# Performance work log

Hardware: AMD Instinct MI355X
Metric: run time of the kernel (lower is better)

## Reference

```python
import jax, jax.numpy as jnp
import numpy as np

# ----- Cl(3,0,1) projective geometric algebra tables (e0^2=0, e1..e3^2=+1) -----
_BLADES = [(), (0,), (1,), (2,), (3,),
           (0, 1), (0, 2), (0, 3), (1, 2), (1, 3), (2, 3),
           (0, 1, 2), (0, 1, 3), (0, 2, 3), (1, 2, 3),
           (0, 1, 2, 3)]
_IDX = {b: i for i, b in enumerate(_BLADES)}

def _blade_mul(a, b):
    lst = list(a) + list(b); sign = 1; n = len(lst)
    for _ in range(n):
        for j in range(n - 1):
            if lst[j] > lst[j + 1]:
                lst[j], lst[j + 1] = lst[j + 1], lst[j]; sign = -sign
    out, i = [], 0
    while i < len(lst):
        if i + 1 < len(lst) and lst[i] == lst[i + 1]:
            if lst[i] == 0:
                return 0, ()
            i += 2
        else:
            out.append(lst[i]); i += 1
    return sign, tuple(out)

_GPn = np.zeros((16, 16, 16), dtype=np.float32)
for _i, _a in enumerate(_BLADES):
    for _j, _b in enumerate(_BLADES):
        _s, _c = _blade_mul(_a, _b)
        if _s:
            _GPn[_i, _j, _IDX[_c]] = _s
GP = jnp.asarray(_GPn)                       # geometric-product structure constants
_gr = np.array([len(b) for b in _BLADES])
_P = np.stack([np.diag((_gr == g).astype(np.float32)) for g in range(5)])  # grade projections
_L0 = _GPn[1].T                               # left-multiplication by e0
BASIS = jnp.asarray(np.concatenate([_P, np.stack([_L0 @ _P[g] for g in range(4)])], 0))  # (9,16,16) equivariant-linear basis
INNER = jnp.asarray(np.array([0.0 if 0 in b else 1.0 for b in _BLADES], np.float32))    # invariant inner-product mask (8 ones)

N_HEADS = 8
_EPS = 1e-6

def equi_linear(mv, s, wmv, wsm, wms, wss):
    # mv: (..., Cin, 16), s: (..., Sin); scalars couple to the grade-0 component
    y_mv = jnp.einsum('oik,kab,...ib->...oa', wmv, BASIS, mv)
    y_mv = y_mv.at[..., 0].add(jnp.einsum('oi,...i->...o', wsm, s))
    y_s = jnp.einsum('oi,...i->...o', wss, s) + jnp.einsum('oi,...i->...o', wms, mv[..., 0])
    return y_mv, y_s

def equi_ln(mv, s):
    f = jnp.mean(jnp.sum(mv * mv * INNER, -1), -1, keepdims=True)  # mean channel norm
    mv = mv / jnp.sqrt(f + _EPS)[..., None]
    s = s / jnp.sqrt(jnp.mean(s * s, -1, keepdims=True) + _EPS)
    return mv, s

def attention(mv, s, wmv, wsm, wms, wss, womv, wosm, woms, woss):
    B, N, C, _ = mv.shape; S = s.shape[-1]; H = N_HEADS
    qkv_mv, qkv_s = equi_linear(mv, s, wmv, wsm, wms, wss)
    q_mv, k_mv, v_mv = [t.reshape(B, N, H, C // H, 16) for t in jnp.split(qkv_mv, 3, axis=-2)]
    q_s, k_s, v_s = [t.reshape(B, N, H, S // H) for t in jnp.split(qkv_s, 3, axis=-1)]
    scale = 1.0 / np.sqrt(8 * (C // H) + S // H)  # 8 invariant comps per mv channel
    scores = (jnp.einsum('bnhci,bmhci->bhnm', q_mv * INNER, k_mv)
              + jnp.einsum('bnhd,bmhd->bhnm', q_s, k_s)) * scale
    a = jax.nn.softmax(scores, axis=-1)
    o_mv = jnp.einsum('bhnm,bmhci->bnhci', a, v_mv).reshape(B, N, C, 16)
    o_s = jnp.einsum('bhnm,bmhd->bnhd', a, v_s).reshape(B, N, S)
    return equi_linear(o_mv, o_s, womv, wosm, woms, woss)

def geo_mlp(mv, s, w1mv, w1sm, w1ms, w1ss, w2mv, w2sm, w2ms, w2ss):
    C = mv.shape[-2]; S = s.shape[-1]
    h_mv, h_s = equi_linear(mv, s, w1mv, w1sm, w1ms, w1ss)  # (...,2C,16), (...,2S)
    gp = jnp.einsum('ijk,...ci,...cj->...ck', GP, h_mv[..., :C, :], h_mv[..., C:, :])
    gp = gp * jax.nn.gelu(gp[..., :1])                       # scalar-gated nonlinearity
    sh = h_s[..., :S] * jax.nn.gelu(h_s[..., S:])
    return equi_linear(gp, sh, w2mv, w2sm, w2ms, w2ss)

def _forward(inputs, win_mv, win_ms, win_bs,
             a_qkv_wmv, a_qkv_wsm, a_qkv_wms, a_qkv_wss,
             a_out_wmv, a_out_wsm, a_out_wms, a_out_wss,
             m1_wmv, m1_wsm, m1_wms, m1_wss,
             m2_wmv, m2_wsm, m2_wms, m2_wss,
             wout_mv, wout_sm):
    B, N, _ = inputs.shape
    # embed_point: coordinates -> trivector components, homogeneous e123 = 1
    mv0 = jnp.zeros((B, N, 1, 16), inputs.dtype)
    mv0 = mv0.at[..., 14].set(1.0)
    mv0 = mv0.at[..., 13].set(-inputs[..., 0:1])
    mv0 = mv0.at[..., 12].set(inputs[..., 1:2])
    mv0 = mv0.at[..., 11].set(-inputs[..., 2:3])
    mv = jnp.einsum('oik,kab,...ib->...oa', win_mv, BASIS, mv0)  # (B,N,C,16)
    s = jnp.einsum('oi,...i->...o', win_ms, mv0[..., 0]) + win_bs  # (B,N,S)
    L = a_qkv_wmv.shape[0]
    for l in range(L):  # loop over structurally-distinct layers only
        n_mv, n_s = equi_ln(mv, s)
        d_mv, d_s = attention(n_mv, n_s, a_qkv_wmv[l], a_qkv_wsm[l], a_qkv_wms[l], a_qkv_wss[l],
                              a_out_wmv[l], a_out_wsm[l], a_out_wms[l], a_out_wss[l])
        mv, s = mv + d_mv, s + d_s
        n_mv, n_s = equi_ln(mv, s)
        d_mv, d_s = geo_mlp(n_mv, n_s, m1_wmv[l], m1_wsm[l], m1_wms[l], m1_wss[l],
                            m2_wmv[l], m2_wsm[l], m2_wms[l], m2_wss[l])
        mv, s = mv + d_mv, s + d_s
    out_mv = jnp.einsum('oik,kab,...ib->...oa', wout_mv, BASIS, mv)  # (B,N,1,16)
    out_mv = out_mv.at[..., 0].add(jnp.einsum('oi,...i->...o', wout_sm, s))
    nodewise = out_mv[..., 0:1]                 # extract_scalar: (B,N,1,1)
    return jnp.mean(nodewise, axis=(-3, -2))    # mean over (points, channels) -> (B,1)

def setup_inputs() -> dict:
    key = jax.random.key(0)
    B, N, C, S, L = 8, 1024, 16, 32, 8
    ks = iter(jax.random.split(key, 32))
    def p(shape, fan):
        return jax.random.normal(next(ks), shape, jnp.float32) / np.sqrt(fan)
    return {
        'inputs': jax.random.normal(next(ks), (B, N, 3), jnp.float32),
        'win_mv': p((C, 1, 9), 9.0),
        'win_ms': p((S, 1), 1.0),
        'win_bs': p((S,), 1.0),
        'a_qkv_wmv': p((L, 3 * C, C, 9), 9.0 * C),
        'a_qkv_wsm': p((L, 3 * C, S), S),
        'a_qkv_wms': p((L, 3 * S, C), C),
        'a_qkv_wss': p((L, 3 * S, S), S),
        'a_out_wmv': p((L, C, C, 9), 9.0 * C),
        'a_out_wsm': p((L, C, S), S),
        'a_out_wms': p((L, S, C), C),
        'a_out_wss': p((L, S, S), S),
        'm1_wmv': p((L, 2 * C, C, 9), 9.0 * C),
        'm1_wsm': p((L, 2 * C, S), S),
        'm1_wms': p((L, 2 * S, C), C),
        'm1_wss': p((L, 2 * S, S), S),
        'm2_wmv': p((L, C, C, 9), 9.0 * C),
        'm2_wsm': p((L, C, S), S),
        'm2_wms': p((L, S, C), C),
        'm2_wss': p((L, S, S), S),
        'wout_mv': p((1, C, 9), 9.0 * C),
        'wout_sm': p((1, S), S),
    }

def reference(inputs, win_mv, win_ms, win_bs,
              a_qkv_wmv, a_qkv_wsm, a_qkv_wms, a_qkv_wss,
              a_out_wmv, a_out_wsm, a_out_wms, a_out_wss,
              m1_wmv, m1_wsm, m1_wms, m1_wss,
              m2_wmv, m2_wsm, m2_wms, m2_wss,
              wout_mv, wout_sm):
    return _forward(inputs, win_mv, win_ms, win_bs,
                    a_qkv_wmv, a_qkv_wsm, a_qkv_wms, a_qkv_wss,
                    a_out_wmv, a_out_wsm, a_out_wms, a_out_wss,
                    m1_wmv, m1_wsm, m1_wms, m1_wss,
                    m2_wmv, m2_wsm, m2_wms, m2_wss,
                    wout_mv, wout_sm)
```

## Files before the change

### kernel.cpp

```cpp
#include <hip/hip_runtime.h>
#include <math.h>

#define BB 8
#define NN 1024
#define LLAYERS 8

typedef unsigned short ushort_t;
typedef unsigned int uint_t;
using bf16x8 = __attribute__((ext_vector_type(8))) short;
using f32x4  = __attribute__((ext_vector_type(4))) float;

__constant__ int d_GRADE[16] = {0,1,1,1,1,2,2,2,2,2,2,3,3,3,3,4};
__constant__ int d_PAIR[16]  = {-1,0,-1,-1,-1,2,3,4,-1,-1,-1,8,9,10,-1,14};
__constant__ int d_IB[8] = {0,2,3,4,8,9,10,14};
__constant__ int d_I2M[16] = {0,1,2,4,8,3,5,9,6,10,12,7,11,13,14,15};
__constant__ int d_M2I[16] = {0,1,2,5,3,6,8,11,4,7,9,12,10,13,14,15};

#define QSCALE (0.22360679774997896f * 1.4426950408889634f)

__device__ __forceinline__ float gelu_tanh(float x) {
  float y = 0.7978845608028654f * (x + 0.044715f * x * x * x);
  float e2 = __builtin_amdgcn_exp2f(y * -2.8853900817779268f);
  return x * __builtin_amdgcn_rcpf(1.0f + e2);
}

__device__ __forceinline__ ushort_t f2b(float f) {
  union { float f; unsigned int u; } x;
  x.f = f;
  unsigned int r = x.u + 0x7fffu + ((x.u >> 16) & 1u);
  return (ushort_t)(r >> 16);
}

__global__ void __launch_bounds__(256) k_embed(
    const float* __restrict__ inp, const float* __restrict__ win_mv,
    const float* __restrict__ win_ms, const float* __restrict__ win_bs,
    float* __restrict__ mv, float* __restrict__ s)
{
  int tok = blockIdx.x, t = threadIdx.x;
  float x = inp[tok * 3 + 0];
  float y = inp[tok * 3 + 1];
  float z = inp[tok * 3 + 2];
  int o = t >> 4, aa = t & 15;
  float ma = (aa == 14) ? 1.f : (aa == 13) ? -x : (aa == 12) ? y : (aa == 11) ? -z : 0.f;
  int g = d_GRADE[aa];
  float val = win_mv[o * 9 + g] * ma;
  int pr = d_PAIR[aa];
  if (pr >= 0) {
    float mp = (pr == 14) ? 1.f : 0.f;
    val += win_mv[o * 9 + 4 + g] * mp;
  }
  mv[(size_t)tok * 256 + t] = val;
  if (t < 32) s[(size_t)tok * 32 + t] = win_bs[t];
  (void)win_ms;
}

__global__ void __launch_bounds__(256) k_ln_qkv(
    const float* __restrict__ mv, const float* __restrict__ s,
    const float* __restrict__ wmv, const float* __restrict__ wsm,
    const float* __restrict__ wms, const float* __restrict__ wss,
    ushort_t* __restrict__ q_bf, ushort_t* __restrict__ k_bf, ushort_t* __restrict__ vT)
{
  __shared__ float pool[9600];
  float* xmv = pool;
  float* xs  = pool + 2048;
  float* yst = pool + 2304;
  float* sst = pool + 8832;

  int t = threadIdx.x;
  int tok0 = blockIdx.x * 8;
  int b = tok0 >> 10, n0 = tok0 & 1023;
  int a = t & 15, og = t >> 4;
  int g = d_GRADE[a], pr = d_PAIR[a];

  float wgq[16], wpq[16], wgk[16], wpk[16], wgv[16], wpv[16];
  #pragma unroll
  for (int i = 0; i < 16; ++i) {
    wgq[i] = wmv[(og)      * 144 + i * 9 + g];
    wgk[i] = wmv[(16 + og) * 144 + i * 9 + g];
    wgv[i] = wmv[(32 + og) * 144 + i * 9 + g];
    wpq[i] = wmv[(og)      * 144 + i * 9 + 4 + g];
    wpk[i] = wmv[(16 + og) * 144 + i * 9 + 4 + g];
    wpv[i] = wmv[(32 + og) * 144 + i * 9 + 4 + g];
  }

  #pragma unroll
  for (int j = 0; j < 2; ++j)
    *(float4*)&xmv[t * 4 + j * 1024] = *(const float4*)&mv[(size_t)tok0 * 256 + t * 4 + j * 1024];
  if (t < 64)
    *(float4*)&xs[t * 4] = *(const float4*)&s[(size_t)tok0 * 32 + t * 4];
  __syncthreads();

  if (t < 128) {
    int tk = t >> 4, ch = t & 15;
    float* xp = &xmv[tk * 256 + ch * 16];
    float4 v0 = *(float4*)&xp[0], v1 = *(float4*)&xp[4];
    float4 v2 = *(float4*)&xp[8], v3 = *(float4*)&xp[12];
    float ss = v0.x*v0.x + v0.z*v0.z + v0.w*v0.w + v1.x*v1.x
             + v2.x*v2.x + v2.y*v2.y + v2.z*v2.z + v3.z*v3.z;
    ss += __shfl_xor(ss, 1); ss += __shfl_xor(ss, 2);
    ss += __shfl_xor(ss, 4); ss += __shfl_xor(ss, 8);
    float inv = rsqrtf(ss / 16.f + 1e-6f);
    v0.x*=inv; v0.y*=inv; v0.z*=inv; v0.w*=inv;
    v1.x*=inv; v1.y*=inv; v1.z*=inv; v1.w*=inv;
    v2.x*=inv; v2.y*=inv; v2.z*=inv; v2.w*=inv;
    v3.x*=inv; v3.y*=inv; v3.z*=inv; v3.w*=inv;
    *(float4*)&xp[0] = v0; *(float4*)&xp[4] = v1;
    *(float4*)&xp[8] = v2; *(float4*)&xp[12] = v3;
    float s0 = xs[tk * 32 + ch * 2], s1 = xs[tk * 32 + ch * 2 + 1];
    float s2 = s0 * s0 + s1 * s1;
    s2 += __shfl_xor(s2, 1); s2 += __shfl_xor(s2, 2);
    s2 += __shfl_xor(s2, 4); s2 += __shfl_xor(s2, 8);
    float sinv = rsqrtf(s2 / 32.f + 1e-6f);
    xs[tk * 32 + ch * 2] = s0 * sinv;
    xs[tk * 32 + ch * 2 + 1] = s1 * sinv;
  }
  __syncthreads();

  for (int tk = 0; tk < 8; ++tk) {
    float y0 = 0.f, y1 = 0.f, y2 = 0.f;
    const float* xb = &xmv[tk * 256];
    #pragma unroll
    for (int i = 0; i < 16; ++i) {
      float xa_ = xb[i * 16 + a];
      y0 += wgq[i] * xa_; y1 += wgk[i] * xa_; y2 += wgv[i] * xa_;
    }
    if (pr >= 0) {
      #pragma unroll
      for (int i = 0; i < 16; ++i) {
        float xp_ = xb[i * 16 + pr];
        y0 += wpq[i] * xp_; y1 += wpk[i] * xp_; y2 += wpv[i] * xp_;
      }
    }
    yst[(tk * 48 + og) * 17 + a] = y0;
    yst[(tk * 48 + 16 + og) * 17 + a] = y1;
    yst[(tk * 48 + 32 + og) * 17 + a] = y2;
  }
  __syncthreads();

  for (int u = t; u < 384; u += 256) {
    int tk = u / 48, o = u % 48;
    float add = 0.f;
    #pragma unroll
    for (int j = 0; j < 32; ++j) add += wsm[o * 32 + j] * xs[tk * 32 + j];
    yst[(tk * 48 + o) * 17 + 0] += add;
  }
  for (int u = t; u < 768; u += 256) {
    int tk = u / 96, o96 = u % 96;
    float yy = 0.f;
    #pragma unroll
    for (int j = 0; j < 32; ++j) yy += wss[o96 * 32 + j] * xs[tk * 32 + j];
    #pragma unroll
    for (int i = 0; i < 16; ++i) yy += wms[o96 * 16 + i] * xmv[tk * 256 + i * 16];
    sst[tk * 96 + o96] = yy;
  }
  __syncthreads();

  if (t < 128) {
    int isK = t >> 6;
    int r = t & 63;
    int tk = r >> 3, h = r & 7;
    float scale = isK ? 1.f : QSCALE;
    const float* base = &yst[(tk * 48 + isK * 16) * 17];
    ushort_t tmp[32];
    #pragma unroll
    for (int j = 0; j < 8; ++j) {
      int blade = d_IB[j];
      tmp[j]     = f2b(base[(2 * h)     * 17 + blade] * scale);
      tmp[8 + j] = f2b(base[(2 * h + 1) * 17 + blade] * scale);
    }
    #pragma unroll
    for (int d = 0; d < 4; ++d)
      tmp[16 + d] = f2b(sst[tk * 96 + isK * 32 + h * 4 + d] * scale);
    #pragma unroll
    for (int j2 = 20; j2 < 32; ++j2) tmp[j2] = 0;
    uint_t out[16];
    #pragma unroll
    for (int j3 = 0; j3 < 16; ++j3)
      out[j3] = (uint_t)tmp[2 * j3] | ((uint_t)tmp[2 * j3 + 1] << 16);
    ushort_t* dst = (isK ? k_bf : q_bf) + ((size_t)(b * 8 + h) * 1024 + n0 + tk) * 32;
    *(uint4*)(dst +  0) = make_uint4(out[0],  out[1],  out[2],  out[3]);
    *(uint4*)(dst +  8) = make_uint4(out[4],  out[5],  out[6],  out[7]);
    *(uint4*)(dst + 16) = make_uint4(out[8],  out[9],  out[10], out[11]);
    *(uint4*)(dst + 24) = make_uint4(out[12], out[13], out[14], out[15]);
  }
  {
    int h = t >> 5, dim = t & 31;
    int ch = 2 * h + (dim >> 4), blade = dim & 15;
    uint_t ov[4];
    #pragma unroll
    for (int tk = 0; tk < 8; ++tk) {
      ushort_t bv = f2b(yst[(tk * 48 + 32 + ch) * 17 + blade]);
      if (tk & 1) ov[tk >> 1] |= ((uint_t)bv) << 16; else ov[tk >> 1] = bv;
    }
    ushort_t* dst = vT + ((size_t)(b * 8 + h) * 48 + dim) * 1024 + n0;
    *(uint4*)dst = make_uint4(ov[0], ov[1], ov[2], ov[3]);
  }
  if (t < 32) {
    int h = t >> 2, d = t & 3;
    uint_t ov[4];
    #pragma unroll
    for (int tk = 0; tk < 8; ++tk) {
      ushort_t bv = f2b(sst[tk * 96 + 64 + h * 4 + d]);
      if (tk & 1) ov[tk >> 1] |= ((uint_t)bv) << 16; else ov[tk >> 1] = bv;
    }
    ushort_t* dst = vT + ((size_t)(b * 8 + h) * 48 + 32 + d) * 1024 + n0;
    *(uint4*)dst = make_uint4(ov[0], ov[1], ov[2], ov[3]);
  }
  if (t < 8) {
    ushort_t* dst = vT + ((size_t)(b * 8 + t) * 48 + 36) * 1024 + n0;
    *(uint4*)dst = make_uint4(0x3F803F80u, 0x3F803F80u, 0x3F803F80u, 0x3F803F80u);
  }
}

#define OPART_STRIDE 2359296
#define LPART_STRIDE 65536
__global__ void __launch_bounds__(256) k_attn(
    const ushort_t* __restrict__ q_bf, const ushort_t* __restrict__ k_bf,
    const ushort_t* __restrict__ vT, float* __restrict__ o_mvA, float* __restrict__ lA)
{
  __shared__ __align__(16) ushort_t kst[64 * 40];
  __shared__ __align__(16) ushort_t vst[48 * 72];
  __shared__ __align__(16) ushort_t plds[4][1280];
  int bx = blockIdx.x;
  int bh = bx & 63, qg = bx >> 6;
  int qb = qg & 15, kg = qg >> 4;
  int b = bh >> 3, h = bh & 7;
  int t = threadIdx.x;
  int w = t >> 6, lane = t & 63;
  int quad = lane >> 4, col = lane & 15;
  int q16 = qb * 64 + w * 16;
  size_t hb = (size_t)bh * 1024;
  ushort_t* myp = &plds[w][0];

  float* o_mvp = o_mvA + (size_t)kg * OPART_STRIDE;
  float* o_sp  = o_mvp + 2097152;
  float* l_p   = lA + (size_t)kg * LPART_STRIDE;

  bf16x8 qfrag = *(const bf16x8*)(q_bf + (hb + q16 + col) * 32 + quad * 8);

  f32x4 ot0 = {0.f,0.f,0.f,0.f}, ot1 = {0.f,0.f,0.f,0.f}, ot2 = {0.f,0.f,0.f,0.f};

  const ushort_t* kbase = k_bf + hb * 32;
  const ushort_t* vbase = vT + (size_t)bh * 48 * 1024;
  int k0 = kg * 512;

  int skey = t >> 2, sc4 = t & 3;
  for (int kt = 0; kt < 8; ++kt) {
    int kb = k0 + kt * 64;
    __syncthreads();
    *(uint4*)&kst[skey * 40 + sc4 * 8] =
        *(const uint4*)(kbase + (size_t)(kb + skey) * 32 + sc4 * 8);
    for (int u = t; u < 296; u += 256) {
      int row = u >> 3, c8 = u & 7;
      *(uint4*)&vst[row * 72 + c8 * 8] =
          *(const uint4*)(vbase + (size_t)row * 1024 + kb + c8 * 8);
    }
    __syncthreads();

    bf16x8 sk0 = *(const bf16x8*)&kst[(     col) * 40 + quad * 8];
    bf16x8 sk1 = *(const bf16x8*)&kst[(16 + col) * 40 + quad * 8];
    bf16x8 sk2 = *(const bf16x8*)&kst[(32 + col) * 40 + quad * 8];
    bf16x8 sk3 = *(const bf16x8*)&kst[(48 + col) * 40 + quad * 8];
    bf16x8 va0 = *(const bf16x8*)&vst[(     col) * 72 + quad * 8];
    bf16x8 va1 = *(const bf16x8*)&vst[(16 + col) * 72 + quad * 8];
    bf16x8 va2 = *(const bf16x8*)&vst[(32 + col) * 72 + quad * 8];
    bf16x8 vb0 = *(const bf16x8*)&vst[(     col) * 72 + 32 + quad * 8];
    bf16x8 vb1 = *(const bf16x8*)&vst[(16 + col) * 72 + 32 + quad * 8];
    bf16x8 vb2 = *(const bf16x8*)&vst[(32 + col) * 72 + 32 + quad * 8];
    f32x4 zero = {0.f,0.f,0.f,0.f};
    f32x4 sa0 = __builtin_amdgcn_mfma_f32_16x16x32_bf16(sk0, qfrag, zero, 0, 0, 0);
    f32x4 sa1 = __builtin_amdgcn_mfma_f32_16x16x32_bf16(sk1, qfrag, zero, 0, 0, 0);
    f32x4 sb0 = __builtin_amdgcn_mfma_f32_16x16x32_bf16(sk2, qfrag, zero, 0, 0, 0);
    f32x4 sb1 = __builtin_amdgcn_mfma_f32_16x16x32_bf16(sk3, qfrag, zero, 0, 0, 0);

    union { float f; uint_t u; } e0, e1, e2, e3;
    e0.f = __builtin_amdgcn_exp2f(sa0[0]); e1.f = __builtin_amdgcn_exp2f(sa0[1]);
    e2.f = __builtin_amdgcn_exp2f(sa0[2]); e3.f = __builtin_amdgcn_exp2f(sa0[3]);
    uint_t a0 = __builtin_amdgcn_perm(e1.u, e0.u, 0x07060302u);
    uint_t a1 = __builtin_amdgcn_perm(e3.u, e2.u, 0x07060302u);
    e0.f = __builtin_amdgcn_exp2f(sa1[0]); e1.f = __builtin_amdgcn_exp2f(sa1[1]);
    e2.f = __builtin_amdgcn_exp2f(sa1[2]); e3.f = __builtin_amdgcn_exp2f(sa1[3]);
    uint_t a2 = __builtin_amdgcn_perm(e1.u, e0.u, 0x07060302u);
    uint_t a3 = __builtin_amdgcn_perm(e3.u, e2.u, 0x07060302u);
    e0.f = __builtin_amdgcn_exp2f(sb0[0]); e1.f = __builtin_amdgcn_exp2f(sb0[1]);
    e2.f = __builtin_amdgcn_exp2f(sb0[2]); e3.f = __builtin_amdgcn_exp2f(sb0[3]);
    uint_t b0 = __builtin_amdgcn_perm(e1.u, e0.u, 0x07060302u);
    uint_t b1 = __builtin_amdgcn_perm(e3.u, e2.u, 0x07060302u);
    e0.f = __builtin_amdgcn_exp2f(sb1[0]); e1.f = __builtin_amdgcn_exp2f(sb1[1]);
    e2.f = __builtin_amdgcn_exp2f(sb1[2]); e3.f = __builtin_amdgcn_exp2f(sb1[3]);
    uint_t b2 = __builtin_amdgcn_perm(e1.u, e0.u, 0x07060302u);
    uint_t b3 = __builtin_amdgcn_perm(e3.u, e2.u, 0x07060302u);

    *(uint2*)(myp + col * 40 + quad * 4)            = make_uint2(a0, a1);
    *(uint2*)(myp + col * 40 + 16 + quad * 4)       = make_uint2(a2, a3);
    *(uint2*)(myp + 640 + col * 40 + quad * 4)      = make_uint2(b0, b1);
    *(uint2*)(myp + 640 + col * 40 + 16 + quad * 4) = make_uint2(b2, b3);
    __builtin_amdgcn_wave_barrier();
    bf16x8 pfa = *(const bf16x8*)(myp + col * 40 + quad * 8);
    bf16x8 pfb = *(const bf16x8*)(myp + 640 + col * 40 + quad * 8);
    __builtin_amdgcn_wave_barrier();
    ot0 = __builtin_amdgcn_mfma_f32_16x16x32_bf16(va0, pfa, ot0, 0, 0, 0);
    ot1 = __builtin_amdgcn_mfma_f32_16x16x32_bf16(va1, pfa, ot1, 0, 0, 0);
    ot2 = __builtin_amdgcn_mfma_f32_16x16x32_bf16(va2, pfa, ot2, 0, 0, 0);
    ot0 = __builtin_amdgcn_mfma_f32_16x16x32_bf16(vb0, pfb, ot0, 0, 0, 0);
    ot1 = __builtin_amdgcn_mfma_f32_16x16x32_bf16(vb1, pfb, ot1, 0, 0, 0);
    ot2 = __builtin_amdgcn_mfma_f32_16x16x32_bf16(vb2, pfb, ot2, 0, 0, 0);
  }

  int tok = b * NN + q16 + col;
  float* op0 = o_mvp + (size_t)tok * 256 + (2 * h) * 16 + quad * 4;
  op0[0] = ot0[0]; op0[1] = ot0[1]; op0[2] = ot0[2]; op0[3] = ot0[3];
  float* op1 = o_mvp + (size_t)tok * 256 + (2 * h + 1) * 16 + quad * 4;
  op1[0] = ot1[0]; op1[1] = ot1[1]; op1[2] = ot1[2]; op1[3] = ot1[3];
  if (quad == 0) {
    float* osp = o_sp + (size_t)tok * 32 + h * 4;
    osp[0] = ot2[0]; osp[1] = ot2[1]; osp[2] = ot2[2]; osp[3] = ot2[3];
  }
  if (quad == 1) l_p[hb + q16 + col] = ot2[0];
}

__global__ void __launch_bounds__(256) k_out_res(
    const float* __restrict__ o_mvA, const float* __restrict__ lA,
    const float* __restrict__ wmv, const float* __restrict__ wsm,
    const float* __restrict__ wms, const float* __restrict__ wss,
    float* __restrict__ mv, float* __restrict__ s)
{
  __shared__ float pool[4544];
  float* xo    = pool;
  float* xso   = pool + 2048;
  float* yst   = pool + 2304;
  float* invls = pool + 4480;

  const float* o_sA  = o_mvA + 2097152;
  const float* o_mvB = o_mvA + OPART_STRIDE;
  const float* o_sB  = o_mvB + 2097152;
  const float* lB    = lA + LPART_STRIDE;

  int t = threadIdx.x;
  int tok0 = blockIdx.x * 8;
  int b8 = (tok0 >> 10) * 8, n0 = tok0 & 1023;
  int a = t & 15, og = t >> 4;
  int g = d_GRADE[a], pr = d_PAIR[a];

  float wg[16], wp[16];
  #pragma unroll
  for (int i = 0; i < 16; ++i) {
    wg[i] = wmv[og * 144 + i * 9 + g];
    wp[i] = wmv[og * 144 + i * 9 + 4 + g];
  }

  float4 ra[2], rc[2];
  #pragma unroll
  for (int j = 0; j < 2; ++j) {
    ra[j] = *(const float4*)&o_mvA[(size_t)tok0 * 256 + t * 4 + j * 1024];
    rc[j] = *(const float4*)&o_mvB[(size_t)tok0 * 256 + t * 4 + j * 1024];
  }
  float4 sa4 = {0,0,0,0}, sc4 = {0,0,0,0};
  if (t < 64) {
    int tk = t >> 3, h = t & 7;
    sa4 = *(const float4*)&o_sA[(size_t)(tok0 + tk) * 32 + h * 4];
    sc4 = *(const float4*)&o_sB[(size_t)(tok0 + tk) * 32 + h * 4];
    float la = lA[(size_t)(b8 + h) * 1024 + n0 + tk];
    float lb = lB[(size_t)(b8 + h) * 1024 + n0 + tk];
    invls[t] = 1.f / (la + lb);
  }
  __syncthreads();

  #pragma unroll
  for (int j = 0; j < 2; ++j) {
    int idx = t * 4 + j * 1024;
    int tk = idx >> 8, o = (idx >> 4) & 15;
    float il = invls[tk * 8 + (o >> 1)];
    xo[idx + 0] = (ra[j].x + rc[j].x) * il;
    xo[idx + 1] = (ra[j].y + rc[j].y) * il;
    xo[idx + 2] = (ra[j].z + rc[j].z) * il;
    xo[idx + 3] = (ra[j].w + rc[j].w) * il;
  }
  if (t < 64) {
    int tk = t >> 3, h = t & 7;
    float il = invls[t];
    xso[tk * 32 + h * 4 + 0] = (sa4.x + sc4.x) * il;
    xso[tk * 32 + h * 4 + 1] = (sa4.y + sc4.y) * il;
    xso[tk * 32 + h * 4 + 2] = (sa4.z + sc4.z) * il;
    xso[tk * 32 + h * 4 + 3] = (sa4.w + sc4.w) * il;
  }
  __syncthreads();

  for (int tk = 0; tk < 8; ++tk) {
    float y = 0.f;
    const float* xb = &xo[tk * 256];
    #pragma unroll
    for (int i = 0; i < 16; ++i) y += wg[i] * xb[i * 16 + a];
    if (pr >= 0) {
      #pragma unroll
      for (int i = 0; i < 16; ++i) y += wp[i] * xb[i * 16 + pr];
    }
    yst[(tk * 16 + og) * 17 + a] = y;
  }
  __syncthreads();

  if (t < 128) {
    int tk = t >> 4, o = t & 15;
    float add = 0.f;
    #pragma unroll
    for (int j = 0; j < 32; ++j) add += wsm[o * 32 + j] * xso[tk * 32 + j];
    yst[(tk * 16 + o) * 17 + 0] += add;
  }
  {
    int o32 = t & 31, tk = t >> 5;
    float ys = 0.f;
    #pragma unroll
    for (int j = 0; j < 32; ++j) ys += wss[o32 * 32 + j] * xso[tk * 32 + j];
    #pragma unroll
    for (int i = 0; i < 16; ++i) ys += wms[o32 * 16 + i] * xo[tk * 256 + i * 16];
    s[(size_t)(tok0 + tk) * 32 + o32] += ys;
  }
  __syncthreads();

  #pragma unroll
  for (int p = 0; p < 8; ++p) {
    int flat = p * 256 + t;
    int tk = flat >> 8, rem = flat & 255, o = rem >> 4, a2 = rem & 15;
    mv[(size_t)tok0 * 256 + flat] += yst[(tk * 16 + o) * 17 + a2];
  }
}

__global__ void __launch_bounds__(256) k_mlp_res(
    float* __restrict__ mv, float* __restrict__ s,
    const float* __restrict__ w1mv, const float* __restrict__ w1sm,
    const float* __restrict__ w1ms, const float* __restrict__ w1ss,
    const float* __restrict__ w2mv, const float* __restrict__ w2sm,
    const float* __restrict__ w2ms, const float* __restrict__ w2ss)
{
  __shared__ float pool[9600];
  float* xmv  = pool;
  float* xs   = pool + 2048;
  float* hst  = pool + 2304;
  float* y2st = pool + 2304;
  float* hsst = pool + 6656;
  float* gst  = pool + 7168;
  float* shst = pool + 9344;

  int t = threadIdx.x;
  int tok0 = blockIdx.x * 8;
  int a = t & 15, og = t >> 4;
  int g = d_GRADE[a], pr = d_PAIR[a];

  unsigned long long jpack = 0; unsigned int spack = 0, skipm = 0;
  {
    int mk = d_I2M[a];
    for (int i = 0; i < 16; ++i) {
      int mi = d_I2M[i];
      int mj = mi ^ mk;
      if (mi & mj & 1) { skipm |= 1u << i; continue; }
      int j = d_M2I[mj];
      int sw = 0;
      for (int bb2 = 0; bb2 < 4; ++bb2)
        if (mj & (1 << bb2)) sw += __popc(((unsigned)mi) >> (bb2 + 1));
      jpack |= (unsigned long long)j << (4 * i);
      spack |= (unsigned)(sw & 1) << i;
    }
  }

  float wg1a[16], wp1a[16], wg1b[16], wp1b[16];
  #pragma unroll
  for (int i = 0; i < 16; ++i) {
    wg1a[i] = w1mv[(og)      * 144 + i * 9 + g];
    wg1b[i] = w1mv[(16 + og) * 144 + i * 9 + g];
    wp1a[i] = w1mv[(og)      * 144 + i * 9 + 4 + g];
    wp1b[i] = w1mv[(16 + og) * 144 + i * 9 + 4 + g];
  }

  #pragma unroll
  for (int j = 0; j < 2; ++j)
    *(float4*)&xmv[t * 4 + j * 1024] = *(const float4*)&mv[(size_t)tok0 * 256 + t * 4 + j * 1024];
  if (t < 64)
    *(float4*)&xs[t * 4] = *(const float4*)&s[(size_t)tok0 * 32 + t * 4];
  __syncthreads();

  if (t < 128) {
    int tk = t >> 4, ch = t & 15;
    float* xp = &xmv[tk * 256 + ch * 16];
    float4 v0 = *(float4*)&xp[0], v1 = *(float4*)&xp[4];
    float4 v2 = *(float4*)&xp[8], v3 = *(float4*)&xp[12];
    float ss = v0.x*v0.x + v0.z*v0.z + v0.w*v0.w + v1.x*v1.x
             + v2.x*v2.x + v2.y*v2.y + v2.z*v2.z + v3.z*v3.z;
    ss += __shfl_xor(ss, 1); ss += __shfl_xor(ss, 2);
    ss += __shfl_xor(ss, 4); ss += __shfl_xor(ss, 8);
    float inv = rsqrtf(ss / 16.f + 1e-6f);
    v0.x*=inv; v0.y*=inv; v0.z*=inv; v0.w*=inv;
    v1.x*=inv; v1.y*=inv; v1.z*=inv; v1.w*=inv;
    v2.x*=inv; v2.y*=inv; v2.z*=inv; v2.w*=inv;
    v3.x*=inv; v3.y*=inv; v3.z*=inv; v3.w*=inv;
    *(float4*)&xp[0] = v0; *(float4*)&xp[4] = v1;
    *(float4*)&xp[8] = v2; *(float4*)&xp[12] = v3;
    float s0 = xs[tk * 32 + ch * 2], s1 = xs[tk * 32 + ch * 2 + 1];
    float s2 = s0 * s0 + s1 * s1;
    s2 += __shfl_xor(s2, 1); s2 += __shfl_xor(s2, 2);
    s2 += __shfl_xor(s2, 4); s2 += __shfl_xor(s2, 8);
    float sinv = rsqrtf(s2 / 32.f + 1e-6f);
    xs[tk * 32 + ch * 2] = s0 * sinv;
    xs[tk * 32 + ch * 2 + 1] = s1 * sinv;
  }
  __syncthreads();

  for (int tk = 0; tk < 8; ++tk) {
    float y0 = 0.f, y1 = 0.f;
    const float* xb = &xmv[tk * 256];
    #pragma unroll
    for (int i = 0; i < 16; ++i) {
      float xa_ = xb[i * 16 + a];
      y0 += wg1a[i] * xa_; y1 += wg1b[i] * xa_;
    }
    if (pr >= 0) {
      #pragma unroll
      for (int i = 0; i < 16; ++i) {
        float xp_ = xb[i * 16 + pr];
        y0 += wp1a[i] * xp_; y1 += wp1b[i] * xp_;
      }
    }
    hst[(tk * 32 + og) * 17 + a] = y0;
    hst[(tk * 32 + 16 + og) * 17 + a] = y1;
  }
  for (int u = t; u < 512; u += 256) {
    int tk = u >> 6, o64 = u & 63;
    float yy = 0.f;
    #pragma unroll
    for (int j = 0; j < 32; ++j) yy += w1ss[o64 * 32 + j] * xs[tk * 32 + j];
    #pragma unroll
    for (int i = 0; i < 16; ++i) yy += w1ms[o64 * 16 + i] * xmv[tk * 256 + i * 16];
    hsst[tk * 64 + o64] = yy;
  }
  __syncthreads();

  {
    int tk = t >> 5, o = t & 31;
    float add = 0.f;
    #pragma unroll
    for (int j = 0; j < 32; ++j) add += w1sm[o * 32 + j] * xs[tk * 32 + j];
    hst[(tk * 32 + o) * 17 + 0] += add;
  }
  __syncthreads();

  for (int tk = 0; tk < 8; ++tk) {
    const float* h1b = &hst[(tk * 32 + og) * 17];
    const float* h2b = &hst[(tk * 32 + 16 + og) * 17];
    float gacc = 0.f;
    #pragma unroll
    for (int i = 0; i < 16; ++i) {
      int j = (int)((jpack >> (4 * i)) & 15ull);
      float val = h1b[i] * h2b[j];
      float sv = ((spack >> i) & 1) ? -val : val;
      gacc += ((skipm >> i) & 1) ? 0.f : sv;
    }
    float gp0 = __shfl(gacc, (int)(t & 48), 64);
    gst[(tk * 16 + og) * 17 + a] = gacc * gelu_tanh(gp0);
  }
  {
    int tk = t >> 5, o32 = t & 31;
    shst[tk * 32 + o32] = hsst[tk * 64 + o32] * gelu_tanh(hsst[tk * 64 + 32 + o32]);
  }
  __syncthreads();

  {
    float wg2[16], wp2[16];
    #pragma unroll
    for (int i = 0; i < 16; ++i) {
      wg2[i] = w2mv[og * 144 + i * 9 + g];
      wp2[i] = w2mv[og * 144 + i * 9 + 4 + g];
    }
    for (int tk = 0; tk < 8; ++tk) {
      float y = 0.f;
      #pragma unroll
      for (int i = 0; i < 16; ++i) y += wg2[i] * gst[(tk * 16 + i) * 17 + a];
      if (pr >= 0) {
        #pragma unroll
        for (int i = 0; i < 16; ++i) y += wp2[i] * gst[(tk * 16 + i) * 17 + pr];
      }
      y2st[(tk * 16 + og) * 17 + a] = y;
    }
  }
  __syncthreads();

  if (t < 128) {
    int tk = t >> 4, o = t & 15;
    float add = 0.f;
    #pragma unroll
    for (int j = 0; j < 32; ++j) add += w2sm[o * 32 + j] * shst[tk * 32 + j];
    y2st[(tk * 16 + o) * 17 + 0] += add;
  }
  {
    int tk = t >> 5, o32 = t & 31;
    float ys = 0.f;
    #pragma unroll
    for (int j = 0; j < 32; ++j) ys += w2ss[o32 * 32 + j] * shst[tk * 32 + j];
    #pragma unroll
    for (int i = 0; i < 16; ++i) ys += w2ms[o32 * 16 + i] * gst[(tk * 16 + i) * 17 + 0];
    s[(size_t)(tok0 + tk) * 32 + o32] += ys;
  }
  __syncthreads();

  #pragma unroll
  for (int p = 0; p < 8; ++p) {
    int flat = p * 256 + t;
    int tk = flat >> 8, rem = flat & 255, o = rem >> 4, a2 = rem & 15;
    mv[(size_t)tok0 * 256 + flat] += y2st[(tk * 16 + o) * 17 + a2];
  }
}

__global__ void __launch_bounds__(256) k_final(
    const float* __restrict__ mv, const float* __restrict__ s,
    const float* __restrict__ wout_mv, const float* __restrict__ wout_sm,
    float* __restrict__ out)
{
  __shared__ float red[256];
  int b = blockIdx.x, t = threadIdx.x;
  float part = 0.f;
  for (int n = t; n < NN; n += 256) {
    const float* mvp = mv + ((size_t)(b * NN + n) * 16) * 16;
    const float* sp = s + (size_t)(b * NN + n) * 32;
    float acc = 0.f;
    #pragma unroll
    for (int i = 0; i < 16; ++i) acc += wout_mv[i * 9] * mvp[i * 16];
    #pragma unroll
    for (int j = 0; j < 32; ++j) acc += wout_sm[j] * sp[j];
    part += acc;
  }
  red[t] = part;
  __syncthreads();
  for (int w = 128; w > 0; w >>= 1) { if (t < w) red[t] += red[t + w]; __syncthreads(); }
  if (t == 0) out[b] = red[0] / (float)NN;
}

extern "C" void kernel_launch(void* const* d_in, const int* in_sizes, int n_in,
                              void* d_out, int out_size, void* d_ws, size_t ws_size,
                              hipStream_t stream) {
  const float* inputs    = (const float*)d_in[0];
  const float* win_mv    = (const float*)d_in[1];
  const float* win_ms    = (const float*)d_in[2];
  const float* win_bs    = (const float*)d_in[3];
  const float* a_qkv_wmv = (const float*)d_in[4];
  const float* a_qkv_wsm = (const float*)d_in[5];
  const float* a_qkv_wms = (const float*)d_in[6];
  const float* a_qkv_wss = (const float*)d_in[7];
  const float* a_out_wmv = (const float*)d_in[8];
  const float* a_out_wsm = (const float*)d_in[9];
  const float* a_out_wms = (const float*)d_in[10];
  const float* a_out_wss = (const float*)d_in[11];
  const float* m1_wmv    = (const float*)d_in[12];
  const float* m1_wsm    = (const float*)d_in[13];
  const float* m1_wms    = (const float*)d_in[14];
  const float* m1_wss    = (const float*)d_in[15];
  const float* m2_wmv    = (const float*)d_in[16];
  const float* m2_wsm    = (const float*)d_in[17];
  const float* m2_wms    = (const float*)d_in[18];
  const float* m2_wss    = (const float*)d_in[19];
  const float* wout_mv   = (const float*)d_in[20];
  const float* wout_sm   = (const float*)d_in[21];
  float* out = (float*)d_out;

  float* ws = (float*)d_ws;
  float* mv    = ws;
  float* s     = mv + 2097152;
  float* o_mvA = s + 262144;
  float* lA    = o_mvA + 2 * 2359296;
  ushort_t* q_bf = (ushort_t*)(lA + 2 * 65536);
  ushort_t* k_bf = q_bf + 2097152;
  ushort_t* vT   = k_bf + 2097152;

  int ntok = BB * NN;
  int ntile = ntok / 8;
  k_embed<<<ntok, 256, 0, stream>>>(inputs, win_mv, win_ms, win_bs, mv, s);

  for (int l = 0; l < LLAYERS; ++l) {
    k_ln_qkv<<<ntile, 256, 0, stream>>>(mv, s,
        a_qkv_wmv + (size_t)l * 48 * 16 * 9, a_qkv_wsm + (size_t)l * 48 * 32,
        a_qkv_wms + (size_t)l * 96 * 16,     a_qkv_wss + (size_t)l * 96 * 32,
        q_bf, k_bf, vT);
    k_attn<<<2048, 256, 0, stream>>>(q_bf, k_bf, vT, o_mvA, lA);
    k_out_res<<<ntile, 256, 0, stream>>>(o_mvA, lA,
        a_out_wmv + (size_t)l * 16 * 16 * 9, a_out_wsm + (size_t)l * 16 * 32,
        a_out_wms + (size_t)l * 32 * 16,     a_out_wss + (size_t)l * 32 * 32,
        mv, s);
    k_mlp_res<<<ntile, 256, 0, stream>>>(mv, s,
        m1_wmv + (size_t)l * 32 * 16 * 9, m1_wsm + (size_t)l * 32 * 32,
        m1_wms + (size_t)l * 64 * 16,     m1_wss + (size_t)l * 64 * 32,
        m2_wmv + (size_t)l * 16 * 16 * 9, m2_wsm + (size_t)l * 16 * 32,
        m2_wms + (size_t)l * 32 * 16,     m2_wss + (size_t)l * 32 * 32);
  }

  k_final<<<BB, 256, 0, stream>>>(mv, s, wout_mv, wout_sm, out);

  (void)in_sizes; (void)n_in; (void)out_size; (void)ws_size;
}
```

Measured before the change: 1.021 ms.

## Restructure MLP residual kernel with transposed shared layout and register-held residuals

The MLP residual kernel now keeps each thread's mv inputs in registers across the whole kernel and computes the layer-norm with wave shuffles plus a small cross-wave reduction. It stores normalized inputs and gated activations transposed with padded rows so the channel contractions read float4 vectors from shared memory. The scalar-to-grade-0 terms are precomputed into small tables, which removes the separate read-modify-write passes and the final staging copy back to global memory. The aim is fewer shared-memory accesses and barriers and a direct residual write. The trade-off is higher register pressure and a more intricate shared-memory aliasing scheme.

```diff
diff --git a/kernel.cpp b/kernel.cpp
--- a/kernel.cpp
+++ b/kernel.cpp
@@ -432,19 +432,23 @@
     const float* __restrict__ w2mv, const float* __restrict__ w2sm,
     const float* __restrict__ w2ms, const float* __restrict__ w2ss)
 {
-  __shared__ float pool[9600];
-  float* xmv  = pool;
-  float* xs   = pool + 2048;
-  float* hst  = pool + 2304;
-  float* y2st = pool + 2304;
-  float* hsst = pool + 6656;
-  float* gst  = pool + 7168;
-  float* shst = pool + 9344;
+  __shared__ __align__(16) float pool[9120];
+  float* xT    = pool;
+  float* gstT  = pool;
+  float* xs    = pool + 2560;
+  float* w1smT = pool + 2816;
+  float* hst   = pool + 3072;
+  float* hsst  = pool + 8192;
+  float* shst  = pool + 8704;
+  float* w2smT = pool + 8960;
+  float* redp  = pool + 9088;
 
   int t = threadIdx.x;
   int tok0 = blockIdx.x * 8;
   int a = t & 15, og = t >> 4;
   int g = d_GRADE[a], pr = d_PAIR[a];
+  int inner_a = ((d_I2M[a] & 1) == 0) ? 1 : 0;
+  int tks = t >> 5, o32 = t & 31;
 
   unsigned long long jpack = 0; unsigned int spack = 0, skipm = 0;
   {
@@ -462,103 +466,137 @@
     }
   }
 
-  float wg1a[16], wp1a[16], wg1b[16], wp1b[16];
-  #pragma unroll
-  for (int i = 0; i < 16; ++i) {
-    wg1a[i] = w1mv[(og)      * 144 + i * 9 + g];
-    wg1b[i] = w1mv[(16 + og) * 144 + i * 9 + g];
-    wp1a[i] = w1mv[(og)      * 144 + i * 9 + 4 + g];
-    wp1b[i] = w1mv[(16 + og) * 144 + i * 9 + 4 + g];
-  }
-
-  #pragma unroll
-  for (int j = 0; j < 2; ++j)
-    *(float4*)&xmv[t * 4 + j * 1024] = *(const float4*)&mv[(size_t)tok0 * 256 + t * 4 + j * 1024];
-  if (t < 64)
-    *(float4*)&xs[t * 4] = *(const float4*)&s[(size_t)tok0 * 32 + t * 4];
-  __syncthreads();
-
-  if (t < 128) {
-    int tk = t >> 4, ch = t & 15;
-    float* xp = &xmv[tk * 256 + ch * 16];
-    float4 v0 = *(float4*)&xp[0], v1 = *(float4*)&xp[4];
-    float4 v2 = *(float4*)&xp[8], v3 = *(float4*)&xp[12];
-    float ss = v0.x*v0.x + v0.z*v0.z + v0.w*v0.w + v1.x*v1.x
-             + v2.x*v2.x + v2.y*v2.y + v2.z*v2.z + v3.z*v3.z;
-    ss += __shfl_xor(ss, 1); ss += __shfl_xor(ss, 2);
-    ss += __shfl_xor(ss, 4); ss += __shfl_xor(ss, 8);
-    float inv = rsqrtf(ss / 16.f + 1e-6f);
-    v0.x*=inv; v0.y*=inv; v0.z*=inv; v0.w*=inv;
-    v1.x*=inv; v1.y*=inv; v1.z*=inv; v1.w*=inv;
-    v2.x*=inv; v2.y*=inv; v2.z*=inv; v2.w*=inv;
-    v3.x*=inv; v3.y*=inv; v3.z*=inv; v3.w*=inv;
-    *(float4*)&xp[0] = v0; *(float4*)&xp[4] = v1;
-    *(float4*)&xp[8] = v2; *(float4*)&xp[12] = v3;
-    float s0 = xs[tk * 32 + ch * 2], s1 = xs[tk * 32 + ch * 2 + 1];
-    float s2 = s0 * s0 + s1 * s1;
+  float mvv[8];
+  #pragma unroll
+  for (int tk = 0; tk < 8; ++tk)
+    mvv[tk] = mv[(size_t)(tok0 + tk) * 256 + t];
+  float sold = s[(size_t)(tok0 + tks) * 32 + o32];
+
+  float sq[8];
+  #pragma unroll
+  for (int tk = 0; tk < 8; ++tk) sq[tk] = inner_a ? mvv[tk] * mvv[tk] : 0.f;
+  #pragma unroll
+  for (int off = 1; off < 64; off <<= 1) {
+    #pragma unroll
+    for (int tk = 0; tk < 8; ++tk) sq[tk] += __shfl_xor(sq[tk], off);
+  }
+  if ((t & 63) == 0) {
+    #pragma unroll
+    for (int tk = 0; tk < 8; ++tk) redp[(t >> 6) * 8 + tk] = sq[tk];
+  }
+  __syncthreads();
+  #pragma unroll
+  for (int tk = 0; tk < 8; ++tk) {
+    float f = redp[tk] + redp[8 + tk] + redp[16 + tk] + redp[24 + tk];
+    float inv = rsqrtf(f / 16.f + 1e-6f);
+    xT[tk * 320 + a * 20 + og] = mvv[tk] * inv;
+  }
+  {
+    float s2 = sold * sold;
     s2 += __shfl_xor(s2, 1); s2 += __shfl_xor(s2, 2);
-    s2 += __shfl_xor(s2, 4); s2 += __shfl_xor(s2, 8);
+    s2 += __shfl_xor(s2, 4); s2 += __shfl_xor(s2, 8); s2 += __shfl_xor(s2, 16);
     float sinv = rsqrtf(s2 / 32.f + 1e-6f);
-    xs[tk * 32 + ch * 2] = s0 * sinv;
-    xs[tk * 32 + ch * 2 + 1] = s1 * sinv;
-  }
-  __syncthreads();
-
-  for (int tk = 0; tk < 8; ++tk) {
-    float y0 = 0.f, y1 = 0.f;
-    const float* xb = &xmv[tk * 256];
+    xs[tks * 32 + o32] = sold * sinv;
+  }
+  __syncthreads();
+
+  {
+    float add = 0.f;
+    #pragma unroll
+    for (int j = 0; j < 32; ++j) add += w1sm[o32 * 32 + j] * xs[tks * 32 + j];
+    w1smT[tks * 32 + o32] = add;
+  }
+  __syncthreads();
+
+  {
+    float wg1a[16], wp1a[16], wg1b[16], wp1b[16];
     #pragma unroll
     for (int i = 0; i < 16; ++i) {
-      float xa_ = xb[i * 16 + a];
-      y0 += wg1a[i] * xa_; y1 += wg1b[i] * xa_;
-    }
-    if (pr >= 0) {
-      #pragma unroll
-      for (int i = 0; i < 16; ++i) {
-        float xp_ = xb[i * 16 + pr];
-        y0 += wp1a[i] * xp_; y1 += wp1b[i] * xp_;
+      wg1a[i] = w1mv[(og)      * 144 + i * 9 + g];
+      wg1b[i] = w1mv[(16 + og) * 144 + i * 9 + g];
+      wp1a[i] = w1mv[(og)      * 144 + i * 9 + 4 + g];
+      wp1b[i] = w1mv[(16 + og) * 144 + i * 9 + 4 + g];
+    }
+    #pragma unroll
+    for (int tk = 0; tk < 8; ++tk) {
+      const float* rowa = &xT[tk * 320 + a * 20];
+      float4 q0 = *(const float4*)(rowa + 0), q1 = *(const float4*)(rowa + 4);
+      float4 q2 = *(const float4*)(rowa + 8), q3 = *(const float4*)(rowa + 12);
+      float y0 = q0.x*wg1a[0]+q0.y*wg1a[1]+q0.z*wg1a[2]+q0.w*wg1a[3]
+               + q1.x*wg1a[4]+q1.y*wg1a[5]+q1.z*wg1a[6]+q1.w*wg1a[7]
+               + q2.x*wg1a[8]+q2.y*wg1a[9]+q2.z*wg1a[10]+q2.w*wg1a[11]
+               + q3.x*wg1a[12]+q3.y*wg1a[13]+q3.z*wg1a[14]+q3.w*wg1a[15];
+      float y1 = q0.x*wg1b[0]+q0.y*wg1b[1]+q0.z*wg1b[2]+q0.w*wg1b[3]
+               + q1.x*wg1b[4]+q1.y*wg1b[5]+q1.z*wg1b[6]+q1.w*wg1b[7]
+               + q2.x*wg1b[8]+q2.y*wg1b[9]+q2.z*wg1b[10]+q2.w*wg1b[11]
+               + q3.x*wg1b[12]+q3.y*wg1b[13]+q3.z*wg1b[14]+q3.w*wg1b[15];
+      if (pr >= 0) {
+        const float* rowp = &xT[tk * 320 + pr * 20];
+        float4 p0 = *(const float4*)(rowp + 0), p1 = *(const float4*)(rowp + 4);
+        float4 p2 = *(const float4*)(rowp + 8), p3 = *(const float4*)(rowp + 12);
+        y0 += p0.x*wp1a[0]+p0.y*wp1a[1]+p0.z*wp1a[2]+p0.w*wp1a[3]
+            + p1.x*wp1a[4]+p1.y*wp1a[5]+p1.z*wp1a[6]+p1.w*wp1a[7]
+            + p2.x*wp1a[8]+p2.y*wp1a[9]+p2.z*wp1a[10]+p2.w*wp1a[11]
+            + p3.x*wp1a[12]+p3.y*wp1a[13]+p3.z*wp1a[14]+p3.w*wp1a[15];
+        y1 += p0.x*wp1b[0]+p0.y*wp1b[1]+p0.z*wp1b[2]+p0.w*wp1b[3]
+            + p1.x*wp1b[4]+p1.y*wp1b[5]+p1.z*wp1b[6]+p1.w*wp1b[7]
+            + p2.x*wp1b[8]+p2.y*wp1b[9]+p2.z*wp1b[10]+p2.w*wp1b[11]
+            + p3.x*wp1b[12]+p3.y*wp1b[13]+p3.z*wp1b[14]+p3.w*wp1b[15];
       }
-    }
-    hst[(tk * 32 + og) * 17 + a] = y0;
-    hst[(tk * 32 + 16 + og) * 17 + a] = y1;
-  }
-  for (int u = t; u < 512; u += 256) {
+      if (a == 0) {
+        y0 += w1smT[tk * 32 + og];
+        y1 += w1smT[tk * 32 + 16 + og];
+      }
+      hst[tk * 640 + og * 20 + a] = y0;
+      hst[tk * 640 + (16 + og) * 20 + a] = y1;
+    }
+  }
+  #pragma unroll
+  for (int p = 0; p < 2; ++p) {
+    int u = p * 256 + t;
     int tk = u >> 6, o64 = u & 63;
     float yy = 0.f;
     #pragma unroll
     for (int j = 0; j < 32; ++j) yy += w1ss[o64 * 32 + j] * xs[tk * 32 + j];
-    #pragma unroll
-    for (int i = 0; i < 16; ++i) yy += w1ms[o64 * 16 + i] * xmv[tk * 256 + i * 16];
+    const float* row0 = &xT[tk * 320];
+    float4 r0 = *(const float4*)(row0 + 0), r1 = *(const float4*)(row0 + 4);
+    float4 r2 = *(const float4*)(row0 + 8), r3 = *(const float4*)(row0 + 12);
+    yy += r0.x*w1ms[o64*16+0]+r0.y*w1ms[o64*16+1]+r0.z*w1ms[o64*16+2]+r0.w*w1ms[o64*16+3]
+        + r1.x*w1ms[o64*16+4]+r1.y*w1ms[o64*16+5]+r1.z*w1ms[o64*16+6]+r1.w*w1ms[o64*16+7]
+        + r2.x*w1ms[o64*16+8]+r2.y*w1ms[o64*16+9]+r2.z*w1ms[o64*16+10]+r2.w*w1ms[o64*16+11]
+        + r3.x*w1ms[o64*16+12]+r3.y*w1ms[o64*16+13]+r3.z*w1ms[o64*16+14]+r3.w*w1ms[o64*16+15];
     hsst[tk * 64 + o64] = yy;
   }
   __syncthreads();
 
-  {
-    int tk = t >> 5, o = t & 31;
-    float add = 0.f;
-    #pragma unroll
-    for (int j = 0; j < 32; ++j) add += w1sm[o * 32 + j] * xs[tk * 32 + j];
-    hst[(tk * 32 + o) * 17 + 0] += add;
-  }
-  __syncthreads();
-
+  #pragma unroll
   for (int tk = 0; tk < 8; ++tk) {
-    const float* h1b = &hst[(tk * 32 + og) * 17];
-    const float* h2b = &hst[(tk * 32 + 16 + og) * 17];
+    const float* row1 = &hst[tk * 640 + og * 20];
+    float4 q0 = *(const float4*)(row1 + 0), q1 = *(const float4*)(row1 + 4);
+    float4 q2 = *(const float4*)(row1 + 8), q3 = *(const float4*)(row1 + 12);
+    float r1[16] = {q0.x,q0.y,q0.z,q0.w, q1.x,q1.y,q1.z,q1.w,
+                    q2.x,q2.y,q2.z,q2.w, q3.x,q3.y,q3.z,q3.w};
+    const float* h2b = &hst[tk * 640 + (16 + og) * 20];
     float gacc = 0.f;
     #pragma unroll
     for (int i = 0; i < 16; ++i) {
       int j = (int)((jpack >> (4 * i)) & 15ull);
-      float val = h1b[i] * h2b[j];
+      float val = r1[i] * h2b[j];
       float sv = ((spack >> i) & 1) ? -val : val;
       gacc += ((skipm >> i) & 1) ? 0.f : sv;
     }
     float gp0 = __shfl(gacc, (int)(t & 48), 64);
-    gst[(tk * 16 + og) * 17 + a] = gacc * gelu_tanh(gp0);
-  }
-  {
-    int tk = t >> 5, o32 = t & 31;
-    shst[tk * 32 + o32] = hsst[tk * 64 + o32] * gelu_tanh(hsst[tk * 64 + 32 + o32]);
+    gstT[tk * 320 + a * 20 + og] = gacc * gelu_tanh(gp0);
+  }
+  shst[tks * 32 + o32] = hsst[tks * 64 + o32] * gelu_tanh(hsst[tks * 64 + 32 + o32]);
+  __syncthreads();
+
+  if (t < 128) {
+    int tk = t >> 4, o = t & 15;
+    float add = 0.f;
+    #pragma unroll
+    for (int j = 0; j < 32; ++j) add += w2sm[o * 32 + j] * shst[tk * 32 + j];
+    w2smT[tk * 16 + o] = add;
   }
   __syncthreads();
 
@@ -569,42 +607,40 @@
       wg2[i] = w2mv[og * 144 + i * 9 + g];
       wp2[i] = w2mv[og * 144 + i * 9 + 4 + g];
     }
+    #pragma unroll
     for (int tk = 0; tk < 8; ++tk) {
-      float y = 0.f;
-      #pragma unroll
-      for (int i = 0; i < 16; ++i) y += wg2[i] * gst[(tk * 16 + i) * 17 + a];
+      const float* rowa = &gstT[tk * 320 + a * 20];
+      float4 q0 = *(const float4*)(rowa + 0), q1 = *(const float4*)(rowa + 4);
+      float4 q2 = *(const float4*)(rowa + 8), q3 = *(const float4*)(rowa + 12);
+      float y = q0.x*wg2[0]+q0.y*wg2[1]+q0.z*wg2[2]+q0.w*wg2[3]
+              + q1.x*wg2[4]+q1.y*wg2[5]+q1.z*wg2[6]+q1.w*wg2[7]
+              + q2.x*wg2[8]+q2.y*wg2[9]+q2.z*wg2[10]+q2.w*wg2[11]
+              + q3.x*wg2[12]+q3.y*wg2[13]+q3.z*wg2[14]+q3.w*wg2[15];
       if (pr >= 0) {
-        #pragma unroll
-        for (int i = 0; i < 16; ++i) y += wp2[i] * gst[(tk * 16 + i) * 17 + pr];
+        const float* rowp = &gstT[tk * 320 + pr * 20];
+        float4 p0 = *(const float4*)(rowp + 0), p1 = *(const float4*)(rowp + 4);
+        float4 p2 = *(const float4*)(rowp + 8), p3 = *(const float4*)(rowp + 12);
+        y += p0.x*wp2[0]+p0.y*wp2[1]+p0.z*wp2[2]+p0.w*wp2[3]
+           + p1.x*wp2[4]+p1.y*wp2[5]+p1.z*wp2[6]+p1.w*wp2[7]
+           + p2.x*wp2[8]+p2.y*wp2[9]+p2.z*wp2[10]+p2.w*wp2[11]
+           + p3.x*wp2[12]+p3.y*wp2[13]+p3.z*wp2[14]+p3.w*wp2[15];
       }
-      y2st[(tk * 16 + og) * 17 + a] = y;
-    }
-  }
-  __syncthreads();
-
-  if (t < 128) {
-    int tk = t >> 4, o = t & 15;
-    float add = 0.f;
-    #pragma unroll
-    for (int j = 0; j < 32; ++j) add += w2sm[o * 32 + j] * shst[tk * 32 + j];
-    y2st[(tk * 16 + o) * 17 + 0] += add;
+      if (a == 0) y += w2smT[tk * 16 + og];
+      mv[(size_t)(tok0 + tk) * 256 + t] = mvv[tk] + y;
+    }
   }
   {
-    int tk = t >> 5, o32 = t & 31;
     float ys = 0.f;
     #pragma unroll
-    for (int j = 0; j < 32; ++j) ys += w2ss[o32 * 32 + j] * shst[tk * 32 + j];
-    #pragma unroll
-    for (int i = 0; i < 16; ++i) ys += w2ms[o32 * 16 + i] * gst[(tk * 16 + i) * 17 + 0];
-    s[(size_t)(tok0 + tk) * 32 + o32] += ys;
-  }
-  __syncthreads();
-
-  #pragma unroll
-  for (int p = 0; p < 8; ++p) {
-    int flat = p * 256 + t;
-    int tk = flat >> 8, rem = flat & 255, o = rem >> 4, a2 = rem & 15;
-    mv[(size_t)tok0 * 256 + flat] += y2st[(tk * 16 + o) * 17 + a2];
+    for (int j = 0; j < 32; ++j) ys += w2ss[o32 * 32 + j] * shst[tks * 32 + j];
+    const float* row0 = &gstT[tks * 320];
+    float4 r0 = *(const float4*)(row0 + 0), r1 = *(const float4*)(row0 + 4);
+    float4 r2 = *(const float4*)(row0 + 8), r3 = *(const float4*)(row0 + 12);
+    ys += r0.x*w2ms[o32*16+0]+r0.y*w2ms[o32*16+1]+r0.z*w2ms[o32*16+2]+r0.w*w2ms[o32*16+3]
+        + r1.x*w2ms[o32*16+4]+r1.y*w2ms[o32*16+5]+r1.z*w2ms[o32*16+6]+r1.w*w2ms[o32*16+7]
+        + r2.x*w2ms[o32*16+8]+r2.y*w2ms[o32*16+9]+r2.z*w2ms[o32*16+10]+r2.w*w2ms[o32*16+11]
+        + r3.x*w2ms[o32*16+12]+r3.y*w2ms[o32*16+13]+r3.z*w2ms[o32*16+14]+r3.w*w2ms[o32*16+15];
+    s[(size_t)(tok0 + tks) * 32 + o32] = sold + ys;
   }
 }
 
```

Result: slower. 1.136 ms (+11.2%).
